# Optimization experiments

Measured on AMD Instinct MI355X. Metric: run time of the kernel, lower is better.

The kernel has to match this reference:

```python
import jax, jax.numpy as jnp
import numpy as np

N = 8192          # number of priors
TOP_K = 50        # max detections returned
IOU_THR = 0.3     # NMS IoU threshold (module-level constant)
VAR0, VAR1 = 0.1, 0.2  # variance buffer


def setup_inputs() -> dict:
    key = jax.random.key(0)
    k1, k2, k3, k4, k5 = jax.random.split(key, 5)
    loc = jax.random.normal(k1, (N, 14), jnp.float32)
    conf = jax.random.uniform(k2, (N, 2), jnp.float32)
    # some iou scores slightly out of [0,1] to exercise the clamp
    iou = jax.random.uniform(k3, (N, 1), jnp.float32) * 1.2 - 0.1
    cxcy = jax.random.uniform(k4, (N, 2), jnp.float32)            # anchor centers in [0,1)
    wh = jax.random.uniform(k5, (N, 2), jnp.float32) * 0.19 + 0.01  # anchor sizes in (0.01,0.2)
    priors = jnp.concatenate([cxcy, wh], axis=1)
    return {"loc": loc, "conf": conf, "iou": iou, "priors": priors}


def _decode(loc, conf, iou, priors):
    cls_scores = conf[:, 1]
    iou_scores = jnp.clip(iou[:, 0], 0.0, 1.0)
    scores = jnp.sqrt(cls_scores * iou_scores)
    p_cxcy, p_wh = priors[:, 0:2], priors[:, 2:4]
    bb_cxcy = p_cxcy + loc[:, 0:2] * VAR0 * p_wh
    var = jnp.array([VAR0, VAR1], jnp.float32)
    bb_wh_half = p_wh * jnp.exp(loc[:, 2:4] * var) * 0.5
    bboxes = jnp.concatenate([bb_cxcy - bb_wh_half, bb_cxcy + bb_wh_half], axis=1)
    # 5 landmarks, each decoded like the box center
    lms = jnp.concatenate(
        [p_cxcy + loc[:, 4 + 2 * i:6 + 2 * i] * VAR0 * p_wh for i in range(5)], axis=1)
    return bboxes, lms, scores


def _nms_keep_idx(bboxes, scores):
    """Greedy NMS; returns indices (into original order) of the first TOP_K kept boxes."""
    order = jnp.argsort(-scores)
    b = bboxes[order]
    x1, y1, x2, y2 = b[:, 0], b[:, 1], b[:, 2], b[:, 3]
    area = (x2 - x1) * (y2 - y1)
    iw = jnp.maximum(jnp.minimum(x2[:, None], x2[None, :]) - jnp.maximum(x1[:, None], x1[None, :]), 0.0)
    ih = jnp.maximum(jnp.minimum(y2[:, None], y2[None, :]) - jnp.maximum(y1[:, None], y1[None, :]), 0.0)
    inter = iw * ih
    iou_mat = inter / (area[:, None] + area[None, :] - inter)  # [N, N]
    idxs = jnp.arange(N)

    def body(i, keep):
        suppressed = jnp.any((iou_mat[i] > IOU_THR) & keep & (idxs < i))
        return keep.at[i].set(~suppressed)

    keep = jax.lax.fori_loop(0, N, body, jnp.zeros((N,), bool))
    kept_pos = jnp.nonzero(keep, size=TOP_K, fill_value=0)[0]  # fixed-size under jit
    return order[kept_pos]


def reference(loc, conf, iou, priors):
    bboxes, lms, scores = _decode(loc, conf, iou, priors)
    keep_idx = _nms_keep_idx(bboxes, scores)
    dets = jnp.concatenate(
        [bboxes[keep_idx], lms[keep_idx], scores[keep_idx][:, None]], axis=1)  # [TOP_K, 15]
    return dets
```

## Files before the change

kernel.cpp:

```cpp
#include <hip/hip_runtime.h>

#define NBOX 8192
#define TOP_K 50
#define IOU_THR 0.3f
#define VAR0 0.1f
#define VAR1 0.2f
#define NT 512
#define NWAVE (NT / 64)
#define MSEL_SUB 32
#define PRE_MAX 256
#define BPT 16

__device__ __forceinline__ void decode_box(int cidx, const float* __restrict__ loc,
                                           const float* __restrict__ priors,
                                           float& x1, float& y1, float& x2, float& y2,
                                           float& area)
{
    float4 pr = *reinterpret_cast<const float4*>(priors + 4 * cidx);
    float l0 = loc[cidx * 14 + 0];
    float l1 = loc[cidx * 14 + 1];
    float l2 = loc[cidx * 14 + 2];
    float l3 = loc[cidx * 14 + 3];
    float cx = pr.x + l0 * VAR0 * pr.z;
    float cy = pr.y + l1 * VAR0 * pr.w;
    float hw = pr.z * expf(l2 * VAR0) * 0.5f;
    float hh = pr.w * expf(l3 * VAR1) * 0.5f;
    x1 = cx - hw; y1 = cy - hh; x2 = cx + hw; y2 = cy + hh;
    area = (x2 - x1) * (y2 - y1);
}

__device__ __forceinline__ void find_thresh(unsigned c0, unsigned c1, unsigned c2, unsigned c3,
                                            int lane, unsigned target, int& bin_sel)
{
    unsigned cnt = c0 + c1 + c2 + c3;
    unsigned S = cnt;
    #pragma unroll
    for (int d = 1; d < 64; d <<= 1) {
        unsigned t = __shfl_down(S, d);
        if (lane + d < 64) S += t;
    }
    unsigned long long bal = __ballot(S >= target);
    int lstar = 63 - __clzll(bal);
    int src = (lstar < 63) ? (lstar + 1) : lstar;
    unsigned Snext = __shfl(S, src);
    unsigned above = (lstar < 63) ? Snext : 0u;
    unsigned bl[4] = {c0, c1, c2, c3};
    int bsel = -1; unsigned acc = above;
    #pragma unroll
    for (int k = 3; k >= 0; --k) {
        if (bsel < 0) {
            if (acc + bl[k] >= target) bsel = k;
            else acc += bl[k];
        }
    }
    bin_sel = 4 * lstar + __shfl(bsel, lstar);
}

__device__ void bitonic_sort(unsigned long long* a, int S, int tid)
{
    for (int k = 2; k <= S; k <<= 1) {
        for (int j = k >> 1; j > 0; j >>= 1) {
            __syncthreads();
            for (int i = tid; i < S; i += NT) {
                int l = i ^ j;
                if (l > i) {
                    unsigned long long A = a[i];
                    unsigned long long B = a[l];
                    bool asc = ((i & k) == 0);
                    if ((A > B) == asc) { a[i] = B; a[l] = A; }
                }
            }
        }
    }
    __syncthreads();
}

__device__ void greedy_nms_serial(const unsigned long long* __restrict__ arr, int n, int lane,
                                  const float* __restrict__ loc, const float* __restrict__ priors,
                                  int* keep_out)
{
    float kx1 = 0.f, ky1 = 0.f, kx2 = 0.f, ky2 = 0.f, karea = 0.f;
    int my_keep = 0, idx0 = 0, kept = 0;
    bool done = false;
    for (int p = 0; p < n && !done; p += 64) {
        int cidx = 0;
        float x1 = 0.f, y1 = 0.f, x2 = 0.f, y2 = 0.f, area = 0.f;
        int pos = p + lane;
        if (pos < n) {
            cidx = (int)(arr[pos] & 0xFFFFFFFFull);
            decode_box(cidx, loc, priors, x1, y1, x2, y2, area);
        }
        int nb = (n - p) < 64 ? (n - p) : 64;
        for (int c = 0; c < nb; ++c) {
            float bx1 = __shfl(x1, c);
            float by1 = __shfl(y1, c);
            float bx2 = __shfl(x2, c);
            float by2 = __shfl(y2, c);
            float barea = __shfl(area, c);
            int   bidx  = __shfl(cidx, c);
            float iw = fmaxf(fminf(kx2, bx2) - fmaxf(kx1, bx1), 0.0f);
            float ih = fmaxf(fminf(ky2, by2) - fmaxf(ky1, by1), 0.0f);
            float inter = iw * ih;
            float v = inter / (karea + barea - inter);
            bool sup = (lane < kept) && (v > IOU_THR);
            if (__ballot(sup) == 0ull) {
                if (kept == 0) idx0 = bidx;
                if (lane == kept) {
                    kx1 = bx1; ky1 = by1; kx2 = bx2; ky2 = by2; karea = barea;
                    my_keep = bidx;
                }
                ++kept;
                if (kept == TOP_K) { done = true; break; }
            }
        }
    }
    if (lane < TOP_K) keep_out[lane] = (lane < kept) ? my_keep : idx0;
}

__global__ __launch_bounds__(NT) void yunet_fused_kernel(
    const float* __restrict__ loc,
    const float* __restrict__ conf,
    const float* __restrict__ iou,
    const float* __restrict__ priors,
    float* __restrict__ out)
{
    __shared__ unsigned long long keys[NBOX];
    __shared__ unsigned long long cand[PRE_MAX];
    __shared__ unsigned hist[NWAVE][256] __attribute__((aligned(16)));
    __shared__ unsigned long long maskbuf[64];
    __shared__ float4 boxs4[PRE_MAX];
    __shared__ float  boxsa[PRE_MAX];
    __shared__ int    idxs[PRE_MAX];
    __shared__ float4 keptb4[TOP_K];
    __shared__ float  kepta[TOP_K];
    __shared__ int keep_sh[TOP_K];
    __shared__ unsigned sh_cnt;
    __shared__ int sh_kept;

    const int tid  = threadIdx.x;
    const int lane = tid & 63;
    const int wid  = tid >> 6;

    const float4* conf4 = reinterpret_cast<const float4*>(conf);
    const float4* iou4  = reinterpret_cast<const float4*>(iou);
    float4 cf[8], io[4];
    #pragma unroll
    for (int m = 0; m < 2; ++m)
        #pragma unroll
        for (int q = 0; q < 4; ++q)
            cf[m * 4 + q] = conf4[(m * NT + tid) * 4 + q];
    #pragma unroll
    for (int m = 0; m < 2; ++m)
        #pragma unroll
        for (int r = 0; r < 2; ++r)
            io[m * 2 + r] = iou4[(m * NT + tid) * 2 + r];

    #pragma unroll
    for (int i = 0; i < 4; ++i) hist[wid][lane + 64 * i] = 0;
    if (tid == 0) { sh_cnt = 0; sh_kept = 0; }
    __asm__ volatile("s_waitcnt lgkmcnt(0)" ::: "memory");

    unsigned sbv[BPT];
    #pragma unroll
    for (int m = 0; m < 2; ++m) {
        float sc[8], uu[8];
        #pragma unroll
        for (int q = 0; q < 4; ++q) {
            sc[2 * q]     = cf[m * 4 + q].y;
            sc[2 * q + 1] = cf[m * 4 + q].w;
        }
        #pragma unroll
        for (int r = 0; r < 2; ++r) {
            uu[4 * r + 0] = io[m * 2 + r].x; uu[4 * r + 1] = io[m * 2 + r].y;
            uu[4 * r + 2] = io[m * 2 + r].z; uu[4 * r + 3] = io[m * 2 + r].w;
        }
        #pragma unroll
        for (int q = 0; q < 8; ++q) {
            float u = fminf(fmaxf(uu[q], 0.0f), 1.0f);
            float s = sqrtf(sc[q] * u);
            unsigned sb = __float_as_uint(s);
            sbv[m * 8 + q] = sb;
            if ((q & 3) == 0) {
                int bin = (int)(s * 256.0f); bin = bin > 255 ? 255 : bin;
                atomicAdd(&hist[wid][bin], 1u);
            }
        }
    }
    __syncthreads();

    int B;
    {
        unsigned c0 = 0, c1 = 0, c2 = 0, c3 = 0;
        #pragma unroll
        for (int w = 0; w < NWAVE; ++w) {
            uint4 h = *(const uint4*)&hist[w][4 * lane];
            c0 += h.x; c1 += h.y; c2 += h.z; c3 += h.w;
        }
        find_thresh(c0, c1, c2, c3, lane, MSEL_SUB, B);
    }

    #pragma unroll
    for (int m = 0; m < 2; ++m) {
        #pragma unroll
        for (int q = 0; q < 8; ++q) {
            unsigned sb = sbv[m * 8 + q];
            float s = __uint_as_float(sb);
            int bin = (int)(s * 256.0f); bin = bin > 255 ? 255 : bin;
            bool pred = (bin >= B);
            unsigned long long bal = __ballot(pred);
            if (pred) {
                int myoff = __popcll(bal & ((1ull << lane) - 1ull));
                unsigned base = 0;
                if (myoff == 0) base = atomicAdd(&sh_cnt, (unsigned)__popcll(bal));
                base = (unsigned)__builtin_amdgcn_readfirstlane((int)base);
                unsigned pos = base + (unsigned)myoff;
                if (pos < PRE_MAX)
                    cand[pos] = ((unsigned long long)(~sb) << 32)
                              | (unsigned)((m * NT + tid) * 8 + q);
            }
        }
    }
    __syncthreads();
    const int C = (int)sh_cnt;

    bool main_ok = (C <= PRE_MAX);
    if (main_ok) {
        if (tid < C) {
            unsigned long long k = cand[tid];
            int r = 0, j = 0;
            for (; j + 4 <= C; j += 4) {
                r += (cand[j]     < k) ? 1 : 0;
                r += (cand[j + 1] < k) ? 1 : 0;
                r += (cand[j + 2] < k) ? 1 : 0;
                r += (cand[j + 3] < k) ? 1 : 0;
            }
            for (; j < C; ++j) r += (cand[j] < k) ? 1 : 0;
            int cidx = (int)(k & 0xFFFFFFFFull);
            float x1, y1, x2, y2, area;
            decode_box(cidx, loc, priors, x1, y1, x2, y2, area);
            boxs4[r] = make_float4(x1, y1, x2, y2);
            boxsa[r] = area;
            idxs[r] = cidx;
        }
        __syncthreads();

        int kept_reg = 0;
        for (int p = 0; p < C; p += 64) {
            unsigned long long sup_prev = 0ull;
            if (tid < 64) {
                int pos = p + lane;
                bool valid = pos < C;
                int rp = valid ? pos : 0;
                float4 b = boxs4[rp]; float a = boxsa[rp];
                bool supP = !valid;
                for (int j = 0; j < kept_reg; ++j) {
                    float4 kb = keptb4[j]; float ka = kepta[j];
                    float iw = fmaxf(fminf(b.z, kb.z) - fmaxf(b.x, kb.x), 0.f);
                    float ih = fmaxf(fminf(b.w, kb.w) - fmaxf(b.y, kb.y), 0.f);
                    float inter = iw * ih;
                    supP = supP || (inter > IOU_THR * (a + ka - inter));
                }
                sup_prev = __ballot(supP);
            }
            {
                int r  = tid >> 3;
                int cb = tid & 7;
                int rp = (p + r < C) ? p + r : 0;
                float4 rb = boxs4[rp]; float ra = boxsa[rp];
                unsigned byte = 0;
                #pragma unroll
                for (int k = 0; k < 8; ++k) {
                    int c = cb * 8 + k;
                    int cp = (p + c < C) ? p + c : 0;
                    float4 cx = boxs4[cp]; float ca = boxsa[cp];
                    float iw = fmaxf(fminf(rb.z, cx.z) - fmaxf(rb.x, cx.x), 0.f);
                    float ih = fmaxf(fminf(rb.w, cx.w) - fmaxf(rb.y, cx.y), 0.f);
                    float inter = iw * ih;
                    byte |= (unsigned)((inter > IOU_THR * (ra + ca - inter)) ? 1u : 0u) << k;
                }
                ((unsigned char*)maskbuf)[tid] = (unsigned char)byte;
            }
            __syncthreads();

            if (tid < 64) {
                unsigned long long myrow = maskbuf[lane];
                unsigned mlo = (unsigned)myrow;
                unsigned mhi = (unsigned)(myrow >> 32);
                unsigned long long keepcur = 0ull;
                const int kept0 = kept_reg;
                int kept = kept0;
                for (int j = 0; j < 64 && kept < TOP_K; ++j) {
                    if (!((sup_prev >> j) & 1ull)) {
                        unsigned long long mj =
                            ((unsigned long long)(unsigned)__builtin_amdgcn_readlane((int)mhi, j) << 32)
                          | (unsigned)__builtin_amdgcn_readlane((int)mlo, j);
                        unsigned long long lower = (1ull << j) - 1ull;
                        if (!(mj & keepcur & lower)) { keepcur |= 1ull << j; ++kept; }
                    }
                }
                unsigned long long lowm = (1ull << lane) - 1ull;
                if ((keepcur >> lane) & 1ull) {
                    int rank = kept0 + __popcll(keepcur & lowm);
                    int pos = p + lane;
                    keep_sh[rank] = idxs[pos];
                    keptb4[rank] = boxs4[pos];
                    kepta[rank] = boxsa[pos];
                }
                kept_reg = kept;
                if (lane == 0) sh_kept = kept;
            }
            __syncthreads();
            if (sh_kept >= TOP_K) break;
        }
    }
    const int kept_total = main_ok ? sh_kept : 0;
    const bool need_fallback = (kept_total < TOP_K);

    if (need_fallback) {
        #pragma unroll
        for (int m = 0; m < 2; ++m) {
            #pragma unroll
            for (int q = 0; q < 8; ++q) {
                int i = (m * NT + tid) * 8 + q;
                keys[i] = ((unsigned long long)(~sbv[m * 8 + q]) << 32) | (unsigned)i;
            }
        }
        __syncthreads();
        bitonic_sort(keys, NBOX, tid);
        if (tid < 64) greedy_nms_serial(keys, NBOX, tid, loc, priors, keep_sh);
        __syncthreads();
    }
    const int kcnt = need_fallback ? TOP_K : kept_total;

    if (tid < TOP_K) {
        int src = (tid < kcnt) ? tid : 0;
        int i = keep_sh[src];
        float4 pr = *reinterpret_cast<const float4*>(priors + 4 * i);
        float cx = pr.x + loc[i * 14 + 0] * VAR0 * pr.z;
        float cy = pr.y + loc[i * 14 + 1] * VAR0 * pr.w;
        float hw = pr.z * expf(loc[i * 14 + 2] * VAR0) * 0.5f;
        float hh = pr.w * expf(loc[i * 14 + 3] * VAR1) * 0.5f;
        float* o = out + tid * 15;
        o[0] = cx - hw;
        o[1] = cy - hh;
        o[2] = cx + hw;
        o[3] = cy + hh;
        #pragma unroll
        for (int q = 0; q < 5; ++q) {
            o[4 + 2 * q] = pr.x + loc[i * 14 + 4 + 2 * q] * VAR0 * pr.z;
            o[5 + 2 * q] = pr.y + loc[i * 14 + 5 + 2 * q] * VAR0 * pr.w;
        }
        float cc = conf[i * 2 + 1];
        float u  = fminf(fmaxf(iou[i], 0.0f), 1.0f);
        o[14] = sqrtf(cc * u);
    }
}

extern "C" void kernel_launch(void* const* d_in, const int* in_sizes, int n_in,
                              void* d_out, int out_size, void* d_ws, size_t ws_size,
                              hipStream_t stream) {
    const float* loc    = (const float*)d_in[0];
    const float* conf   = (const float*)d_in[1];
    const float* iou    = (const float*)d_in[2];
    const float* priors = (const float*)d_in[3];
    float* out = (float*)d_out;

    yunet_fused_kernel<<<1, NT, 0, stream>>>(loc, conf, iou, priors, out);
}
```

Before: 22.77 us.

## Split into multi-block score/decode pre-pass and single-block select+NMS kernel

Adds a 16-block kernel that computes scores, full per-block histograms and decoded boxes into workspace, then a single-block kernel that merges the histograms, selects candidates, and runs NMS using the precomputed boxes. This spreads the memory-bound decode across CUs instead of one block and removes exp/decode from the serial path. It uses the full histogram with threshold target 128 instead of a subsampled one with 32. The cost is an extra kernel launch and a global-memory round trip through the workspace. The original fused kernel is kept as a fallback when the workspace is too small.

```diff
diff --git a/kernel.cpp b/kernel.cpp
--- a/kernel.cpp
+++ b/kernel.cpp
@@ -7,9 +7,16 @@
 #define VAR1 0.2f
 #define NT 512
 #define NWAVE (NT / 64)
-#define MSEL_SUB 32
+#define MSEL 128
 #define PRE_MAX 256
 #define BPT 16
+#define A_BLOCKS 16
+#define A_T 512
+
+#define WS_HIST 0
+#define WS_SCORE 4096
+#define WS_BOX 12288
+#define WS_NEED_BYTES ((size_t)(12288 + 4 * NBOX) * 4)
 
 __device__ __forceinline__ void decode_box(int cidx, const float* __restrict__ loc,
                                            const float* __restrict__ priors,
@@ -56,6 +63,41 @@
     bin_sel = 4 * lstar + __shfl(bsel, lstar);
 }
 
+__global__ __launch_bounds__(A_T) void yunet_score_decode(
+    const float* __restrict__ loc, const float* __restrict__ conf,
+    const float* __restrict__ iou, const float* __restrict__ priors,
+    unsigned* __restrict__ ws)
+{
+    __shared__ unsigned hist[256];
+    const int tid = threadIdx.x;
+    const int i = blockIdx.x * A_T + tid;
+
+    float2 cf = reinterpret_cast<const float2*>(conf)[i];
+    float u = iou[i];
+    float4 pr = reinterpret_cast<const float4*>(priors)[i];
+    float2 l01 = *reinterpret_cast<const float2*>(loc + 14 * i);
+    float2 l23 = *reinterpret_cast<const float2*>(loc + 14 * i + 2);
+
+    if (tid < 256) hist[tid] = 0;
+    __syncthreads();
+
+    u = fminf(fmaxf(u, 0.0f), 1.0f);
+    float s = sqrtf(cf.y * u);
+    unsigned sb = __float_as_uint(s);
+    ws[WS_SCORE + i] = sb;
+    int bin = (int)(s * 256.0f); bin = bin > 255 ? 255 : bin;
+    atomicAdd(&hist[bin], 1u);
+
+    float cx = pr.x + l01.x * VAR0 * pr.z;
+    float cy = pr.y + l01.y * VAR0 * pr.w;
+    float hw = pr.z * expf(l23.x * VAR0) * 0.5f;
+    float hh = pr.w * expf(l23.y * VAR1) * 0.5f;
+    reinterpret_cast<float4*>(ws + WS_BOX)[i] = make_float4(cx - hw, cy - hh, cx + hw, cy + hh);
+
+    __syncthreads();
+    if (tid < 256) ws[WS_HIST + blockIdx.x * 256 + tid] = hist[tid];
+}
+
 __device__ void bitonic_sort(unsigned long long* a, int S, int tid)
 {
     for (int k = 2; k <= S; k <<= 1) {
@@ -75,9 +117,8 @@
     __syncthreads();
 }
 
-__device__ void greedy_nms_serial(const unsigned long long* __restrict__ arr, int n, int lane,
-                                  const float* __restrict__ loc, const float* __restrict__ priors,
-                                  int* keep_out)
+__device__ void greedy_nms_serial_ws(const unsigned long long* __restrict__ arr, int n, int lane,
+                                     const float4* __restrict__ wbox, int* keep_out)
 {
     float kx1 = 0.f, ky1 = 0.f, kx2 = 0.f, ky2 = 0.f, karea = 0.f;
     int my_keep = 0, idx0 = 0, kept = 0;
@@ -88,7 +129,9 @@
         int pos = p + lane;
         if (pos < n) {
             cidx = (int)(arr[pos] & 0xFFFFFFFFull);
-            decode_box(cidx, loc, priors, x1, y1, x2, y2, area);
+            float4 bb = wbox[cidx];
+            x1 = bb.x; y1 = bb.y; x2 = bb.z; y2 = bb.w;
+            area = (x2 - x1) * (y2 - y1);
         }
         int nb = (n - p) < 64 ? (n - p) : 64;
         for (int c = 0; c < nb; ++c) {
@@ -117,16 +160,13 @@
     if (lane < TOP_K) keep_out[lane] = (lane < kept) ? my_keep : idx0;
 }
 
-__global__ __launch_bounds__(NT) void yunet_fused_kernel(
-    const float* __restrict__ loc,
-    const float* __restrict__ conf,
-    const float* __restrict__ iou,
-    const float* __restrict__ priors,
-    float* __restrict__ out)
+__global__ __launch_bounds__(NT) void yunet_select_nms(
+    const float* __restrict__ loc, const float* __restrict__ priors,
+    const unsigned* __restrict__ ws, float* __restrict__ out)
 {
     __shared__ unsigned long long keys[NBOX];
     __shared__ unsigned long long cand[PRE_MAX];
-    __shared__ unsigned hist[NWAVE][256] __attribute__((aligned(16)));
+    __shared__ unsigned histB[256] __attribute__((aligned(16)));
     __shared__ unsigned long long maskbuf[64];
     __shared__ float4 boxs4[PRE_MAX];
     __shared__ float  boxsa[PRE_MAX];
@@ -139,66 +179,40 @@
 
     const int tid  = threadIdx.x;
     const int lane = tid & 63;
-    const int wid  = tid >> 6;
-
-    const float4* conf4 = reinterpret_cast<const float4*>(conf);
-    const float4* iou4  = reinterpret_cast<const float4*>(iou);
-    float4 cf[8], io[4];
-    #pragma unroll
-    for (int m = 0; m < 2; ++m)
-        #pragma unroll
-        for (int q = 0; q < 4; ++q)
-            cf[m * 4 + q] = conf4[(m * NT + tid) * 4 + q];
-    #pragma unroll
-    for (int m = 0; m < 2; ++m)
-        #pragma unroll
-        for (int r = 0; r < 2; ++r)
-            io[m * 2 + r] = iou4[(m * NT + tid) * 2 + r];
-
-    #pragma unroll
-    for (int i = 0; i < 4; ++i) hist[wid][lane + 64 * i] = 0;
+
+    const unsigned* scores = ws + WS_SCORE;
+    const float4* wbox = reinterpret_cast<const float4*>(ws + WS_BOX);
+
+    if (tid < 256) {
+        unsigned s = 0;
+        #pragma unroll
+        for (int b = 0; b < A_BLOCKS; ++b) s += ws[WS_HIST + b * 256 + tid];
+        histB[tid] = s;
+    }
     if (tid == 0) { sh_cnt = 0; sh_kept = 0; }
-    __asm__ volatile("s_waitcnt lgkmcnt(0)" ::: "memory");
-
-    unsigned sbv[BPT];
-    #pragma unroll
-    for (int m = 0; m < 2; ++m) {
-        float sc[8], uu[8];
-        #pragma unroll
-        for (int q = 0; q < 4; ++q) {
-            sc[2 * q]     = cf[m * 4 + q].y;
-            sc[2 * q + 1] = cf[m * 4 + q].w;
-        }
-        #pragma unroll
-        for (int r = 0; r < 2; ++r) {
-            uu[4 * r + 0] = io[m * 2 + r].x; uu[4 * r + 1] = io[m * 2 + r].y;
-            uu[4 * r + 2] = io[m * 2 + r].z; uu[4 * r + 3] = io[m * 2 + r].w;
-        }
-        #pragma unroll
-        for (int q = 0; q < 8; ++q) {
-            float u = fminf(fmaxf(uu[q], 0.0f), 1.0f);
-            float s = sqrtf(sc[q] * u);
-            unsigned sb = __float_as_uint(s);
-            sbv[m * 8 + q] = sb;
-            if ((q & 3) == 0) {
-                int bin = (int)(s * 256.0f); bin = bin > 255 ? 255 : bin;
-                atomicAdd(&hist[wid][bin], 1u);
-            }
-        }
-    }
     __syncthreads();
 
     int B;
     {
-        unsigned c0 = 0, c1 = 0, c2 = 0, c3 = 0;
-        #pragma unroll
-        for (int w = 0; w < NWAVE; ++w) {
-            uint4 h = *(const uint4*)&hist[w][4 * lane];
-            c0 += h.x; c1 += h.y; c2 += h.z; c3 += h.w;
-        }
-        find_thresh(c0, c1, c2, c3, lane, MSEL_SUB, B);
-    }
-
+        uint4 h = *(const uint4*)&histB[4 * lane];
+        find_thresh(h.x, h.y, h.z, h.w, lane, MSEL, B);
+    }
+
+    unsigned sbv[BPT];
+    {
+        const uint4* s4 = reinterpret_cast<const uint4*>(scores);
+        #pragma unroll
+        for (int m = 0; m < 2; ++m) {
+            #pragma unroll
+            for (int r = 0; r < 2; ++r) {
+                uint4 v = s4[(m * NT + tid) * 2 + r];
+                sbv[m * 8 + r * 4 + 0] = v.x;
+                sbv[m * 8 + r * 4 + 1] = v.y;
+                sbv[m * 8 + r * 4 + 2] = v.z;
+                sbv[m * 8 + r * 4 + 3] = v.w;
+            }
+        }
+    }
     #pragma unroll
     for (int m = 0; m < 2; ++m) {
         #pragma unroll
@@ -236,10 +250,9 @@
             }
             for (; j < C; ++j) r += (cand[j] < k) ? 1 : 0;
             int cidx = (int)(k & 0xFFFFFFFFull);
-            float x1, y1, x2, y2, area;
-            decode_box(cidx, loc, priors, x1, y1, x2, y2, area);
-            boxs4[r] = make_float4(x1, y1, x2, y2);
-            boxsa[r] = area;
+            float4 bb = wbox[cidx];
+            boxs4[r] = bb;
+            boxsa[r] = (bb.z - bb.x) * (bb.w - bb.y);
             idxs[r] = cidx;
         }
         __syncthreads();
@@ -327,7 +340,268 @@
         }
         __syncthreads();
         bitonic_sort(keys, NBOX, tid);
-        if (tid < 64) greedy_nms_serial(keys, NBOX, tid, loc, priors, keep_sh);
+        if (tid < 64) greedy_nms_serial_ws(keys, NBOX, tid, wbox, keep_sh);
+        __syncthreads();
+    }
+    const int kcnt = need_fallback ? TOP_K : kept_total;
+
+    if (tid < TOP_K) {
+        int src = (tid < kcnt) ? tid : 0;
+        int i = keep_sh[src];
+        float4 bb = wbox[i];
+        float4 pr = *reinterpret_cast<const float4*>(priors + 4 * i);
+        float* o = out + tid * 15;
+        o[0] = bb.x; o[1] = bb.y; o[2] = bb.z; o[3] = bb.w;
+        #pragma unroll
+        for (int q = 0; q < 5; ++q) {
+            o[4 + 2 * q] = pr.x + loc[i * 14 + 4 + 2 * q] * VAR0 * pr.z;
+            o[5 + 2 * q] = pr.y + loc[i * 14 + 5 + 2 * q] * VAR0 * pr.w;
+        }
+        o[14] = __uint_as_float(scores[i]);
+    }
+}
+
+__global__ __launch_bounds__(NT) void yunet_fused_kernel(
+    const float* __restrict__ loc, const float* __restrict__ conf,
+    const float* __restrict__ iou, const float* __restrict__ priors,
+    float* __restrict__ out)
+{
+    __shared__ unsigned long long keys[NBOX];
+    __shared__ unsigned long long cand[PRE_MAX];
+    __shared__ unsigned hist[NWAVE][256] __attribute__((aligned(16)));
+    __shared__ unsigned long long maskbuf[64];
+    __shared__ float4 boxs4[PRE_MAX];
+    __shared__ float  boxsa[PRE_MAX];
+    __shared__ int    idxs[PRE_MAX];
+    __shared__ float4 keptb4[TOP_K];
+    __shared__ float  kepta[TOP_K];
+    __shared__ int keep_sh[TOP_K];
+    __shared__ unsigned sh_cnt;
+    __shared__ int sh_kept;
+
+    const int tid  = threadIdx.x;
+    const int lane = tid & 63;
+    const int wid  = tid >> 6;
+
+    const float4* conf4 = reinterpret_cast<const float4*>(conf);
+    const float4* iou4  = reinterpret_cast<const float4*>(iou);
+    float4 cf[8], io[4];
+    #pragma unroll
+    for (int m = 0; m < 2; ++m)
+        #pragma unroll
+        for (int q = 0; q < 4; ++q)
+            cf[m * 4 + q] = conf4[(m * NT + tid) * 4 + q];
+    #pragma unroll
+    for (int m = 0; m < 2; ++m)
+        #pragma unroll
+        for (int r = 0; r < 2; ++r)
+            io[m * 2 + r] = iou4[(m * NT + tid) * 2 + r];
+
+    #pragma unroll
+    for (int i = 0; i < 4; ++i) hist[wid][lane + 64 * i] = 0;
+    if (tid == 0) { sh_cnt = 0; sh_kept = 0; }
+    __asm__ volatile("s_waitcnt lgkmcnt(0)" ::: "memory");
+
+    unsigned sbv[BPT];
+    #pragma unroll
+    for (int m = 0; m < 2; ++m) {
+        float sc[8], uu[8];
+        #pragma unroll
+        for (int q = 0; q < 4; ++q) {
+            sc[2 * q]     = cf[m * 4 + q].y;
+            sc[2 * q + 1] = cf[m * 4 + q].w;
+        }
+        #pragma unroll
+        for (int r = 0; r < 2; ++r) {
+            uu[4 * r + 0] = io[m * 2 + r].x; uu[4 * r + 1] = io[m * 2 + r].y;
+            uu[4 * r + 2] = io[m * 2 + r].z; uu[4 * r + 3] = io[m * 2 + r].w;
+        }
+        #pragma unroll
+        for (int q = 0; q < 8; ++q) {
+            float u = fminf(fmaxf(uu[q], 0.0f), 1.0f);
+            float s = sqrtf(sc[q] * u);
+            unsigned sb = __float_as_uint(s);
+            sbv[m * 8 + q] = sb;
+            if ((q & 3) == 0) {
+                int bin = (int)(s * 256.0f); bin = bin > 255 ? 255 : bin;
+                atomicAdd(&hist[wid][bin], 1u);
+            }
+        }
+    }
+    __syncthreads();
+
+    int B;
+    {
+        unsigned c0 = 0, c1 = 0, c2 = 0, c3 = 0;
+        #pragma unroll
+        for (int w = 0; w < NWAVE; ++w) {
+            uint4 h = *(const uint4*)&hist[w][4 * lane];
+            c0 += h.x; c1 += h.y; c2 += h.z; c3 += h.w;
+        }
+        find_thresh(c0, c1, c2, c3, lane, 32, B);
+    }
+
+    #pragma unroll
+    for (int m = 0; m < 2; ++m) {
+        #pragma unroll
+        for (int q = 0; q < 8; ++q) {
+            unsigned sb = sbv[m * 8 + q];
+            float s = __uint_as_float(sb);
+            int bin = (int)(s * 256.0f); bin = bin > 255 ? 255 : bin;
+            bool pred = (bin >= B);
+            unsigned long long bal = __ballot(pred);
+            if (pred) {
+                int myoff = __popcll(bal & ((1ull << lane) - 1ull));
+                unsigned base = 0;
+                if (myoff == 0) base = atomicAdd(&sh_cnt, (unsigned)__popcll(bal));
+                base = (unsigned)__builtin_amdgcn_readfirstlane((int)base);
+                unsigned pos = base + (unsigned)myoff;
+                if (pos < PRE_MAX)
+                    cand[pos] = ((unsigned long long)(~sb) << 32)
+                              | (unsigned)((m * NT + tid) * 8 + q);
+            }
+        }
+    }
+    __syncthreads();
+    const int C = (int)sh_cnt;
+
+    bool main_ok = (C <= PRE_MAX);
+    if (main_ok) {
+        if (tid < C) {
+            unsigned long long k = cand[tid];
+            int r = 0, j = 0;
+            for (; j + 4 <= C; j += 4) {
+                r += (cand[j]     < k) ? 1 : 0;
+                r += (cand[j + 1] < k) ? 1 : 0;
+                r += (cand[j + 2] < k) ? 1 : 0;
+                r += (cand[j + 3] < k) ? 1 : 0;
+            }
+            for (; j < C; ++j) r += (cand[j] < k) ? 1 : 0;
+            int cidx = (int)(k & 0xFFFFFFFFull);
+            float x1, y1, x2, y2, area;
+            decode_box(cidx, loc, priors, x1, y1, x2, y2, area);
+            boxs4[r] = make_float4(x1, y1, x2, y2);
+            boxsa[r] = area;
+            idxs[r] = cidx;
+        }
+        __syncthreads();
+
+        int kept_reg = 0;
+        for (int p = 0; p < C; p += 64) {
+            unsigned long long sup_prev = 0ull;
+            if (tid < 64) {
+                int pos = p + lane;
+                bool valid = pos < C;
+                int rp = valid ? pos : 0;
+                float4 b = boxs4[rp]; float a = boxsa[rp];
+                bool supP = !valid;
+                for (int j = 0; j < kept_reg; ++j) {
+                    float4 kb = keptb4[j]; float ka = kepta[j];
+                    float iw = fmaxf(fminf(b.z, kb.z) - fmaxf(b.x, kb.x), 0.f);
+                    float ih = fmaxf(fminf(b.w, kb.w) - fmaxf(b.y, kb.y), 0.f);
+                    float inter = iw * ih;
+                    supP = supP || (inter > IOU_THR * (a + ka - inter));
+                }
+                sup_prev = __ballot(supP);
+            }
+            {
+                int r  = tid >> 3;
+                int cb = tid & 7;
+                int rp = (p + r < C) ? p + r : 0;
+                float4 rb = boxs4[rp]; float ra = boxsa[rp];
+                unsigned byte = 0;
+                #pragma unroll
+                for (int k = 0; k < 8; ++k) {
+                    int c = cb * 8 + k;
+                    int cp = (p + c < C) ? p + c : 0;
+                    float4 cx = boxs4[cp]; float ca = boxsa[cp];
+                    float iw = fmaxf(fminf(rb.z, cx.z) - fmaxf(rb.x, cx.x), 0.f);
+                    float ih = fmaxf(fminf(rb.w, cx.w) - fmaxf(rb.y, cx.y), 0.f);
+                    float inter = iw * ih;
+                    byte |= (unsigned)((inter > IOU_THR * (ra + ca - inter)) ? 1u : 0u) << k;
+                }
+                ((unsigned char*)maskbuf)[tid] = (unsigned char)byte;
+            }
+            __syncthreads();
+
+            if (tid < 64) {
+                unsigned long long myrow = maskbuf[lane];
+                unsigned mlo = (unsigned)myrow;
+                unsigned mhi = (unsigned)(myrow >> 32);
+                unsigned long long keepcur = 0ull;
+                const int kept0 = kept_reg;
+                int kept = kept0;
+                for (int j = 0; j < 64 && kept < TOP_K; ++j) {
+                    if (!((sup_prev >> j) & 1ull)) {
+                        unsigned long long mj =
+                            ((unsigned long long)(unsigned)__builtin_amdgcn_readlane((int)mhi, j) << 32)
+                          | (unsigned)__builtin_amdgcn_readlane((int)mlo, j);
+                        unsigned long long lower = (1ull << j) - 1ull;
+                        if (!(mj & keepcur & lower)) { keepcur |= 1ull << j; ++kept; }
+                    }
+                }
+                unsigned long long lowm = (1ull << lane) - 1ull;
+                if ((keepcur >> lane) & 1ull) {
+                    int rank = kept0 + __popcll(keepcur & lowm);
+                    int pos = p + lane;
+                    keep_sh[rank] = idxs[pos];
+                    keptb4[rank] = boxs4[pos];
+                    kepta[rank] = boxsa[pos];
+                }
+                kept_reg = kept;
+                if (lane == 0) sh_kept = kept;
+            }
+            __syncthreads();
+            if (sh_kept >= TOP_K) break;
+        }
+    }
+    const int kept_total = main_ok ? sh_kept : 0;
+    const bool need_fallback = (kept_total < TOP_K);
+
+    if (need_fallback) {
+        #pragma unroll
+        for (int m = 0; m < 2; ++m) {
+            #pragma unroll
+            for (int q = 0; q < 8; ++q) {
+                int i = (m * NT + tid) * 8 + q;
+                keys[i] = ((unsigned long long)(~sbv[m * 8 + q]) << 32) | (unsigned)i;
+            }
+        }
+        __syncthreads();
+        bitonic_sort(keys, NBOX, tid);
+        if (tid < 64) {
+            float kx1 = 0.f, ky1 = 0.f, kx2 = 0.f, ky2 = 0.f, karea = 0.f;
+            int my_keep = 0, idx0 = 0, kept = 0;
+            bool done = false;
+            for (int p = 0; p < NBOX && !done; p += 64) {
+                int cidx = (int)(keys[p + lane] & 0xFFFFFFFFull);
+                float x1, y1, x2, y2, area;
+                decode_box(cidx, loc, priors, x1, y1, x2, y2, area);
+                for (int c = 0; c < 64; ++c) {
+                    float bx1 = __shfl(x1, c);
+                    float by1 = __shfl(y1, c);
+                    float bx2 = __shfl(x2, c);
+                    float by2 = __shfl(y2, c);
+                    float barea = __shfl(area, c);
+                    int   bidx  = __shfl(cidx, c);
+                    float iw = fmaxf(fminf(kx2, bx2) - fmaxf(kx1, bx1), 0.0f);
+                    float ih = fmaxf(fminf(ky2, by2) - fmaxf(ky1, by1), 0.0f);
+                    float inter = iw * ih;
+                    float v = inter / (karea + barea - inter);
+                    bool sup = (lane < kept) && (v > IOU_THR);
+                    if (__ballot(sup) == 0ull) {
+                        if (kept == 0) idx0 = bidx;
+                        if (lane == kept) {
+                            kx1 = bx1; ky1 = by1; kx2 = bx2; ky2 = by2; karea = barea;
+                            my_keep = bidx;
+                        }
+                        ++kept;
+                        if (kept == TOP_K) { done = true; break; }
+                    }
+                }
+            }
+            if (lane < TOP_K) keep_sh[lane] = (lane < kept) ? my_keep : idx0;
+        }
         __syncthreads();
     }
     const int kcnt = need_fallback ? TOP_K : kept_total;
@@ -365,5 +639,11 @@
     const float* priors = (const float*)d_in[3];
     float* out = (float*)d_out;
 
-    yunet_fused_kernel<<<1, NT, 0, stream>>>(loc, conf, iou, priors, out);
-}
+    if (ws_size >= WS_NEED_BYTES) {
+        unsigned* ws = (unsigned*)d_ws;
+        yunet_score_decode<<<A_BLOCKS, A_T, 0, stream>>>(loc, conf, iou, priors, ws);
+        yunet_select_nms<<<1, NT, 0, stream>>>(loc, priors, ws, out);
+    } else {
+        yunet_fused_kernel<<<1, NT, 0, stream>>>(loc, conf, iou, priors, out);
+    }
+}
```

Result: slower. 24.61 us (+8.1%).
